# Optimization experiments

Hardware: AMD Instinct MI355X
Metric: run time of the kernel (lower is better)

The kernel has to match this reference:

```python
import jax, jax.numpy as jnp
import numpy as np

B, L, D = 4, 2048, 1024
H = 16
HD = D // H  # head_dim = 64
BASE = 10000.0


def rope_cos_sin(seq_len, head_dim, dtype=jnp.float32):
    inv_freq = 1.0 / (BASE ** (jnp.arange(0, head_dim, 2, dtype=jnp.float32) / head_dim))
    t = jnp.arange(seq_len, dtype=jnp.float32)
    freqs = jnp.outer(t, inv_freq)  # [L, HD/2]
    return jnp.cos(freqs).astype(dtype), jnp.sin(freqs).astype(dtype)


def apply_rope(x, cos, sin):
    # x: [B, H, L, HD]; cos/sin: [L, HD/2]
    x1 = x[..., ::2]
    x2 = x[..., 1::2]
    c = cos[None, None, :, :]
    s = sin[None, None, :, :]
    # NOTE: original concatenates halves (does not re-interleave)
    return jnp.concatenate([x1 * c - x2 * s, x1 * s + x2 * c], axis=-1)


def setup_inputs() -> dict:
    key = jax.random.key(0)
    k1, k2, k3 = jax.random.split(key, 3)
    x = jax.random.normal(k1, (B, L, D), dtype=jnp.float32)
    W_qkv = jax.random.normal(k2, (3 * D, D), dtype=jnp.float32) * (D ** -0.5)
    W_proj = jax.random.normal(k3, (D, D), dtype=jnp.float32) * (D ** -0.5)
    return {"x": x, "W_qkv": W_qkv, "W_proj": W_proj}


def reference(x, W_qkv, W_proj):
    b, l, d = x.shape
    scale = HD ** -0.5
    qkv = jnp.einsum('bld,ed->ble', x, W_qkv)            # [B, L, 3D]
    qkv = qkv.reshape(b, l, 3, H, HD)
    q, k, v = (jnp.transpose(qkv[:, :, i], (0, 2, 1, 3)) for i in range(3))  # [B,H,L,HD]
    cos, sin = rope_cos_sin(l, HD, x.dtype)
    q = apply_rope(q, cos, sin)
    k = apply_rope(k, cos, sin)
    attn = jnp.einsum('bhqd,bhkd->bhqk', q, k) * scale   # [B,H,L,L]
    attn = jax.nn.softmax(attn, axis=-1)
    out = jnp.einsum('bhqk,bhkd->bhqd', attn, v)         # [B,H,L,HD]
    out = jnp.transpose(out, (0, 2, 1, 3)).reshape(b, l, d)
    return jnp.einsum('bld,ed->ble', out, W_proj)
```

## Files before the change

kernel.cpp:

```cpp
#include <hip/hip_runtime.h>
#include <hip/hip_bf16.h>

typedef unsigned short u16;
typedef unsigned int u32;
typedef __attribute__((ext_vector_type(8))) short bf16x8;
typedef __attribute__((ext_vector_type(4))) float f32x4;

#define NL 2048
#define NH 16

__device__ __forceinline__ float bf2f(u16 v) {
    union { float f; unsigned u; } x; x.u = ((unsigned)v) << 16; return x.f;
}
__device__ __forceinline__ u16 f2bf(float f) {
    union { __hip_bfloat16 h; u16 u; } x; x.h = __float2bfloat16(f); return x.u;
}
__device__ __forceinline__ u32 pk2(float a, float b) {
    union { float f; u32 u; } x, y; x.f = a; y.f = b;
    return ((x.u + 0x8000u) >> 16) | ((y.u + 0x8000u) & 0xffff0000u);
}
__device__ __forceinline__ u32 pkt(float lo, float hi) {
    union { float f; u32 u; } x, y; x.f = lo; y.f = hi;
    return __builtin_amdgcn_perm(y.u, x.u, 0x07060302u);
}
#if __has_builtin(__builtin_amdgcn_exp2f)
#define EXP2F(x) __builtin_amdgcn_exp2f(x)
#else
#define EXP2F(x) __expf((x) * 0.69314718056f)
#endif

__device__ __forceinline__ void gload_lds16(const u16* g, u16* l) {
    __builtin_amdgcn_global_load_lds(
        (__attribute__((address_space(1))) void*)(g),
        (__attribute__((address_space(3))) void*)(l), 16, 0, 0);
}

__global__ __launch_bounds__(256) void cast_all_k(const float* __restrict__ x,
                                                  const float* __restrict__ wq,
                                                  const float* __restrict__ wp,
                                                  u16* __restrict__ xo,
                                                  u16* __restrict__ wqo,
                                                  u16* __restrict__ wpo) {
    int i = blockIdx.x * 256 + threadIdx.x;
    const float* src; u16* dst; int off;
    if (i < 2097152)      { src = x;  dst = xo;  off = i; }
    else if (i < 2883584) { src = wq; dst = wqo; off = i - 2097152; }
    else                  { src = wp; dst = wpo; off = i - 2883584; }
    float4 v = *(const float4*)&src[(size_t)off * 4];
    u16 tmp[4] = {f2bf(v.x), f2bf(v.y), f2bf(v.z), f2bf(v.w)};
    *(ushort4*)&dst[(size_t)off * 4] = *(ushort4*)tmp;
}

__global__ __launch_bounds__(256) void rope_table_k(float* __restrict__ cosT,
                                                    float* __restrict__ sinT) {
    int idx = blockIdx.x * 256 + threadIdx.x;
    int l = idx >> 5, i = idx & 31;
    float invf = exp2f(-(float)i * 0.41524101186092029f);
    float ang = (float)l * invf;
    cosT[idx] = cosf(ang);
    sinT[idx] = sinf(ang);
}

template <typename OutT>
__global__ __launch_bounds__(256) void gemm_bt(const u16* __restrict__ A,
                                               const u16* __restrict__ Bm,
                                               OutT* __restrict__ C,
                                               int M, int N, int K) {
    __shared__ u16 As[128][64];
    __shared__ u16 Bs[128][64];
    const int t = threadIdx.x;
    const int lane = t & 63, wave = t >> 6;
    const int quad = lane >> 4, lrow = lane & 15;
    const int wr = wave >> 1, wc = wave & 1;
    const size_t m0 = (size_t)blockIdx.y * 128, n0 = (size_t)blockIdx.x * 128;

    const int srow = wave * 32 + (lane >> 3);
    const int scg  = (lane & 7) ^ (lane >> 3);

    f32x4 acc[4][4];
#pragma unroll
    for (int i = 0; i < 4; ++i)
#pragma unroll
        for (int j = 0; j < 4; ++j) acc[i][j] = (f32x4)0.0f;

    for (int k0 = 0; k0 < K; k0 += 64) {
#pragma unroll
        for (int j = 0; j < 4; ++j) {
            gload_lds16(&A[(m0 + srow + j * 8) * K + k0 + scg * 8],
                        &As[wave * 32 + j * 8][0]);
            gload_lds16(&Bm[(n0 + srow + j * 8) * K + k0 + scg * 8],
                        &Bs[wave * 32 + j * 8][0]);
        }
        __syncthreads();
#pragma unroll
        for (int ks = 0; ks < 2; ++ks) {
            bf16x8 av[4], bv[4];
#pragma unroll
            for (int i = 0; i < 4; ++i)
                av[i] = *(const bf16x8*)
                    &As[wr * 64 + i * 16 + lrow][(((ks << 2) | quad) ^ (lrow & 7)) << 3];
#pragma unroll
            for (int j = 0; j < 4; ++j)
                bv[j] = *(const bf16x8*)
                    &Bs[wc * 64 + j * 16 + lrow][(((ks << 2) | quad) ^ (lrow & 7)) << 3];
#pragma unroll
            for (int i = 0; i < 4; ++i)
#pragma unroll
                for (int j = 0; j < 4; ++j)
                    acc[i][j] = __builtin_amdgcn_mfma_f32_16x16x32_bf16(
                        av[i], bv[j], acc[i][j], 0, 0, 0);
        }
        __syncthreads();
    }
#pragma unroll
    for (int i = 0; i < 4; ++i)
#pragma unroll
        for (int r = 0; r < 4; ++r) {
            size_t row = m0 + wr * 64 + i * 16 + quad * 4 + r;
#pragma unroll
            for (int j = 0; j < 4; ++j) {
                size_t col = n0 + wc * 64 + j * 16 + lrow;
                if constexpr (sizeof(OutT) == 4)
                    C[row * N + col] = acc[i][j][r];
                else
                    C[row * N + col] = f2bf(acc[i][j][r]);
            }
        }
}

__global__ __launch_bounds__(256) void rope_vt_k(const u16* __restrict__ qkv,
                                                 const float* __restrict__ cosT,
                                                 const float* __restrict__ sinT,
                                                 u16* __restrict__ Q,
                                                 u16* __restrict__ Ko,
                                                 u16* __restrict__ VT) {
    __shared__ u16 vtile[64][72];
    const int lt = blockIdx.x, bh = blockIdx.y;
    const int b = bh >> 4, h = bh & 15;
    const int l0 = lt * 64;
    const int t = threadIdx.x;
    const float SC = 0.180336879f;
#pragma unroll
    for (int c = 0; c < 2; ++c) {
        int flat8 = c * 256 + t;
        int li = flat8 >> 3, dg = flat8 & 7;
        const u16* rowp = qkv + (size_t)(b * NL + l0 + li) * 3072 + h * 64 + dg * 8;
        uint4 qv = *(const uint4*)rowp;
        uint4 kv = *(const uint4*)(rowp + 1024);
        uint4 vv = *(const uint4*)(rowp + 2048);
        *(uint4*)&vtile[li][dg * 8] = vv;
        float4 cs = *(const float4*)&cosT[(l0 + li) * 32 + dg * 4];
        float4 sn = *(const float4*)&sinT[(l0 + li) * 32 + dg * 4];
        union { float f; u32 u; } w;
        float e0, o0, e1, o1, e2, o2, e3, o3;
        w.u = qv.x << 16; e0 = w.f; w.u = qv.x & 0xffff0000u; o0 = w.f;
        w.u = qv.y << 16; e1 = w.f; w.u = qv.y & 0xffff0000u; o1 = w.f;
        w.u = qv.z << 16; e2 = w.f; w.u = qv.z & 0xffff0000u; o2 = w.f;
        w.u = qv.w << 16; e3 = w.f; w.u = qv.w & 0xffff0000u; o3 = w.f;
        float c0 = cs.x * SC, c1 = cs.y * SC, c2 = cs.z * SC, c3 = cs.w * SC;
        float s0 = sn.x * SC, s1 = sn.y * SC, s2 = sn.z * SC, s3 = sn.w * SC;
        size_t ob = ((size_t)(b * NH + h) * NL + l0 + li) * 64;
        *(uint2*)&Q[ob + dg * 4] =
            make_uint2(pk2(e0 * c0 - o0 * s0, e1 * c1 - o1 * s1),
                       pk2(e2 * c2 - o2 * s2, e3 * c3 - o3 * s3));
        *(uint2*)&Q[ob + 32 + dg * 4] =
            make_uint2(pk2(e0 * s0 + o0 * c0, e1 * s1 + o1 * c1),
                       pk2(e2 * s2 + o2 * c2, e3 * s3 + o3 * c3));
        float f0, g0, f1, g1, f2, g2, f3, g3;
        w.u = kv.x << 16; f0 = w.f; w.u = kv.x & 0xffff0000u; g0 = w.f;
        w.u = kv.y << 16; f1 = w.f; w.u = kv.y & 0xffff0000u; g1 = w.f;
        w.u = kv.z << 16; f2 = w.f; w.u = kv.z & 0xffff0000u; g2 = w.f;
        w.u = kv.w << 16; f3 = w.f; w.u = kv.w & 0xffff0000u; g3 = w.f;
        *(uint2*)&Ko[ob + dg * 4] =
            make_uint2(pk2(f0 * cs.x - g0 * sn.x, f1 * cs.y - g1 * sn.y),
                       pk2(f2 * cs.z - g2 * sn.z, f3 * cs.w - g3 * sn.w));
        *(uint2*)&Ko[ob + 32 + dg * 4] =
            make_uint2(pk2(f0 * sn.x + g0 * cs.x, f1 * sn.y + g1 * cs.y),
                       pk2(f2 * sn.z + g2 * cs.z, f3 * sn.w + g3 * cs.w));
    }
    __syncthreads();
#pragma unroll
    for (int c = 0; c < 2; ++c) {
        int flat8 = c * 256 + t;
        int d = flat8 >> 3, lg = flat8 & 7;
        u16 tmp[8];
#pragma unroll
        for (int e = 0; e < 8; ++e) tmp[e] = vtile[lg * 8 + e][d];
        *(uint4*)&VT[((size_t)(bh * 64 + d)) * NL + l0 + lg * 8] = *(uint4*)tmp;
    }
}

__global__ __launch_bounds__(512, 6) void attn_k(const u16* __restrict__ Q,
                                                 const u16* __restrict__ Kg,
                                                 const u16* __restrict__ VT,
                                                 u16* __restrict__ Og) {
    __shared__ __align__(16) char smem[49152];
    u16 (*KsB)[64][64] = (u16(*)[64][64])(smem);
    u16 (*VsB)[64][64] = (u16(*)[64][64])(smem + 16384);
    u16* PsBase = (u16*)(smem + 32768);
    const int t = threadIdx.x;
    const int lane = t & 63, wave = t >> 6;
    const int quad = lane >> 4, lq = lane & 15;
    u16* PsW = PsBase + wave * 1024;

    const int qt = blockIdx.x, bh = blockIdx.y;
    const int q0 = qt * 128;
    const size_t qkbase = (size_t)bh * NL * 64;

    const int rsub = lane >> 3;
    const int scg  = (lane & 7) ^ rsub;

    u16 (*Qtmp)[64] = (u16(*)[64])(smem + 32768);
#pragma unroll
    for (int j = 0; j < 2; ++j)
        gload_lds16(&Q[qkbase + (size_t)(q0 + wave * 16 + j * 8 + rsub) * 64 + scg * 8],
                    &Qtmp[wave * 16 + j * 8][0]);
    const u16* kptr = Kg + qkbase + (size_t)(wave * 8 + rsub) * 64 + scg * 8;
    const u16* vptr = VT + qkbase + (size_t)(wave * 8 + rsub) * NL + scg * 8;
    gload_lds16(kptr, &KsB[0][wave * 8][0]);
    gload_lds16(vptr, &VsB[0][wave * 8][0]);
    kptr += 64 * 64;
    vptr += 64;
    __syncthreads();
    bf16x8 bq[2];
#pragma unroll
    for (int ks = 0; ks < 2; ++ks)
        bq[ks] = *(const bf16x8*)&Qtmp[wave * 16 + lq][(((ks << 2) | quad) ^ (lq & 7)) << 3];

    const bf16x8 ones = (bf16x8)(short)16256;
    f32x4 ot[4];
#pragma unroll
    for (int mt = 0; mt < 4; ++mt) ot[mt] = (f32x4)0.0f;
    f32x4 lacc = (f32x4)0.0f;

    for (int kc = 0; kc < NL / 64; ++kc) {
        __syncthreads();
        if (kc < NL / 64 - 1) {
            gload_lds16(kptr, &KsB[(kc + 1) & 1][wave * 8][0]);
            gload_lds16(vptr, &VsB[(kc + 1) & 1][wave * 8][0]);
            kptr += 64 * 64;
            vptr += 64;
        }
        const int cur = kc & 1;

        f32x4 st[4];
#pragma unroll
        for (int mt = 0; mt < 4; ++mt) st[mt] = (f32x4)0.0f;
#pragma unroll
        for (int ks = 0; ks < 2; ++ks)
#pragma unroll
            for (int mt = 0; mt < 4; ++mt) {
                bf16x8 ak = *(const bf16x8*)
                    &KsB[cur][mt * 16 + lq][(((ks << 2) | quad) ^ (lq & 7)) << 3];
                st[mt] = __builtin_amdgcn_mfma_f32_16x16x32_bf16(ak, bq[ks], st[mt], 0, 0, 0);
            }

#pragma unroll
        for (int mt = 0; mt < 4; ++mt) {
            int pblk = (mt * 2 + (quad >> 1)) ^ (lq & 7);
            *(uint2*)&PsW[lq * 64 + pblk * 8 + (quad & 1) * 4] =
                make_uint2(pkt(EXP2F(st[mt][0]), EXP2F(st[mt][1])),
                           pkt(EXP2F(st[mt][2]), EXP2F(st[mt][3])));
        }
        __builtin_amdgcn_s_waitcnt(0xc07f);

#pragma unroll
        for (int ks = 0; ks < 2; ++ks) {
            bf16x8 bp = *(const bf16x8*)
                &PsW[lq * 64 + ((((ks << 2) | quad)) ^ (lq & 7)) * 8];
            lacc = __builtin_amdgcn_mfma_f32_16x16x32_bf16(ones, bp, lacc, 0, 0, 0);
#pragma unroll
            for (int mt = 0; mt < 4; ++mt) {
                bf16x8 av = *(const bf16x8*)
                    &VsB[cur][mt * 16 + lq][(((ks << 2) | quad) ^ (lq & 7)) << 3];
                ot[mt] = __builtin_amdgcn_mfma_f32_16x16x32_bf16(av, bp, ot[mt], 0, 0, 0);
            }
        }
    }

    __syncthreads();
    float* OT_ls = (float*)(smem + wave * 4352);
    float* Ls_ls = (float*)(smem + 34816);
#pragma unroll
    for (int mt = 0; mt < 4; ++mt)
#pragma unroll
        for (int r = 0; r < 4; ++r)
            OT_ls[(mt * 16 + quad * 4 + r) * 17 + lq] = ot[mt][r];
    if (quad == 0) Ls_ls[wave * 16 + lq] = lacc[0];
    __builtin_amdgcn_s_waitcnt(0xc07f);

    const int qq = lane >> 2, dblk = lane & 3;
    float rls = 1.0f / Ls_ls[wave * 16 + qq];
    u16 tmp[16];
#pragma unroll
    for (int e = 0; e < 16; ++e)
        tmp[e] = f2bf(OT_ls[(dblk * 16 + e) * 17 + qq] * rls);
    const int b = bh >> 4, h = bh & 15;
    size_t orow = (size_t)b * NL + q0 + wave * 16 + qq;
    size_t obase = orow * 1024 + h * 64 + dblk * 16;
    *(uint4*)&Og[obase] = *(uint4*)&tmp[0];
    *(uint4*)&Og[obase + 8] = *(uint4*)&tmp[8];
}

extern "C" void kernel_launch(void* const* d_in, const int* in_sizes, int n_in,
                              void* d_out, int out_size, void* d_ws, size_t ws_size,
                              hipStream_t stream) {
    const float* x     = (const float*)d_in[0];
    const float* Wqkv  = (const float*)d_in[1];
    const float* Wproj = (const float*)d_in[2];
    float* out = (float*)d_out;

    char* ws = (char*)d_ws;
    u16* qkv     = (u16*)ws;
    u16* attnout = (u16*)ws;
    u16* Qw      = (u16*)(ws + 50331648);
    u16* Kw      = (u16*)(ws + 67108864);
    u16* VTw     = (u16*)(ws + 83886080);
    float* cosT  = (float*)(ws + 100663296);
    float* sinT  = (float*)(ws + 100925440);
    u16* x_bf    = (u16*)(ws + 101187584);
    u16* Wqkv_bf = (u16*)(ws + 117964800);
    u16* Wproj_bf= (u16*)(ws + 124256256);

    rope_table_k<<<256, 256, 0, stream>>>(cosT, sinT);
    cast_all_k<<<12288, 256, 0, stream>>>(x, Wqkv, Wproj, x_bf, Wqkv_bf, Wproj_bf);
    gemm_bt<u16><<<dim3(24, 64), 256, 0, stream>>>(x_bf, Wqkv_bf, qkv, 8192, 3072, 1024);
    rope_vt_k<<<dim3(32, 64), 256, 0, stream>>>(qkv, cosT, sinT, Qw, Kw, VTw);
    attn_k<<<dim3(16, 64), 512, 0, stream>>>(Qw, Kw, VTw, attnout);
    gemm_bt<float><<<dim3(8, 64), 256, 0, stream>>>(attnout, Wproj_bf, out, 8192, 1024, 1024);
}
```

Measured before the change: 280.1 us.

## Process two query tiles per wave in attention to reuse K/V fragments

Each wave now handles 32 query rows as two 16-row halves instead of 16 rows. Each K and V fragment read from LDS feeds MFMAs for both halves, which halves LDS traffic per MFMA and halves the number of K/V tiles streamed per query. The query tile per block doubles to 256, so the grid shrinks to 512 blocks. LDS grows to 64KB and the launch-bound occupancy hint drops from 6 to 4, which may reduce latency hiding and CU balance.

```diff
diff --git a/kernel.cpp b/kernel.cpp
--- a/kernel.cpp
+++ b/kernel.cpp
@@ -190,21 +190,21 @@
     }
 }
 
-__global__ __launch_bounds__(512, 6) void attn_k(const u16* __restrict__ Q,
+__global__ __launch_bounds__(512, 4) void attn_k(const u16* __restrict__ Q,
                                                  const u16* __restrict__ Kg,
                                                  const u16* __restrict__ VT,
                                                  u16* __restrict__ Og) {
-    __shared__ __align__(16) char smem[49152];
+    __shared__ __align__(16) char smem[65536];
     u16 (*KsB)[64][64] = (u16(*)[64][64])(smem);
     u16 (*VsB)[64][64] = (u16(*)[64][64])(smem + 16384);
     u16* PsBase = (u16*)(smem + 32768);
     const int t = threadIdx.x;
     const int lane = t & 63, wave = t >> 6;
     const int quad = lane >> 4, lq = lane & 15;
-    u16* PsW = PsBase + wave * 1024;
+    u16* PsW = PsBase + wave * 2048;
 
     const int qt = blockIdx.x, bh = blockIdx.y;
-    const int q0 = qt * 128;
+    const int q0 = qt * 256;
     const size_t qkbase = (size_t)bh * NL * 64;
 
     const int rsub = lane >> 3;
@@ -212,9 +212,9 @@
 
     u16 (*Qtmp)[64] = (u16(*)[64])(smem + 32768);
 #pragma unroll
-    for (int j = 0; j < 2; ++j)
-        gload_lds16(&Q[qkbase + (size_t)(q0 + wave * 16 + j * 8 + rsub) * 64 + scg * 8],
-                    &Qtmp[wave * 16 + j * 8][0]);
+    for (int j = 0; j < 4; ++j)
+        gload_lds16(&Q[qkbase + (size_t)(q0 + wave * 32 + j * 8 + rsub) * 64 + scg * 8],
+                    &Qtmp[wave * 32 + j * 8][0]);
     const u16* kptr = Kg + qkbase + (size_t)(wave * 8 + rsub) * 64 + scg * 8;
     const u16* vptr = VT + qkbase + (size_t)(wave * 8 + rsub) * NL + scg * 8;
     gload_lds16(kptr, &KsB[0][wave * 8][0]);
@@ -222,16 +222,21 @@
     kptr += 64 * 64;
     vptr += 64;
     __syncthreads();
-    bf16x8 bq[2];
-#pragma unroll
-    for (int ks = 0; ks < 2; ++ks)
-        bq[ks] = *(const bf16x8*)&Qtmp[wave * 16 + lq][(((ks << 2) | quad) ^ (lq & 7)) << 3];
+    bf16x8 bq[2][2];
+#pragma unroll
+    for (int qh = 0; qh < 2; ++qh)
+#pragma unroll
+        for (int ks = 0; ks < 2; ++ks)
+            bq[qh][ks] = *(const bf16x8*)
+                &Qtmp[wave * 32 + qh * 16 + lq][(((ks << 2) | quad) ^ (lq & 7)) << 3];
 
     const bf16x8 ones = (bf16x8)(short)16256;
-    f32x4 ot[4];
-#pragma unroll
-    for (int mt = 0; mt < 4; ++mt) ot[mt] = (f32x4)0.0f;
-    f32x4 lacc = (f32x4)0.0f;
+    f32x4 ot[2][4];
+#pragma unroll
+    for (int qh = 0; qh < 2; ++qh)
+#pragma unroll
+        for (int mt = 0; mt < 4; ++mt) ot[qh][mt] = (f32x4)0.0f;
+    f32x4 lacc[2] = {(f32x4)0.0f, (f32x4)0.0f};
 
     for (int kc = 0; kc < NL / 64; ++kc) {
         __syncthreads();
@@ -243,37 +248,45 @@
         }
         const int cur = kc & 1;
 
-        f32x4 st[4];
-#pragma unroll
-        for (int mt = 0; mt < 4; ++mt) st[mt] = (f32x4)0.0f;
+        f32x4 st[2][4];
+#pragma unroll
+        for (int qh = 0; qh < 2; ++qh)
+#pragma unroll
+            for (int mt = 0; mt < 4; ++mt) st[qh][mt] = (f32x4)0.0f;
 #pragma unroll
         for (int ks = 0; ks < 2; ++ks)
 #pragma unroll
             for (int mt = 0; mt < 4; ++mt) {
                 bf16x8 ak = *(const bf16x8*)
                     &KsB[cur][mt * 16 + lq][(((ks << 2) | quad) ^ (lq & 7)) << 3];
-                st[mt] = __builtin_amdgcn_mfma_f32_16x16x32_bf16(ak, bq[ks], st[mt], 0, 0, 0);
+                st[0][mt] = __builtin_amdgcn_mfma_f32_16x16x32_bf16(ak, bq[0][ks], st[0][mt], 0, 0, 0);
+                st[1][mt] = __builtin_amdgcn_mfma_f32_16x16x32_bf16(ak, bq[1][ks], st[1][mt], 0, 0, 0);
             }
 
 #pragma unroll
-        for (int mt = 0; mt < 4; ++mt) {
-            int pblk = (mt * 2 + (quad >> 1)) ^ (lq & 7);
-            *(uint2*)&PsW[lq * 64 + pblk * 8 + (quad & 1) * 4] =
-                make_uint2(pkt(EXP2F(st[mt][0]), EXP2F(st[mt][1])),
-                           pkt(EXP2F(st[mt][2]), EXP2F(st[mt][3])));
-        }
+        for (int qh = 0; qh < 2; ++qh)
+#pragma unroll
+            for (int mt = 0; mt < 4; ++mt) {
+                int pblk = (mt * 2 + (quad >> 1)) ^ (lq & 7);
+                *(uint2*)&PsW[(qh * 16 + lq) * 64 + pblk * 8 + (quad & 1) * 4] =
+                    make_uint2(pkt(EXP2F(st[qh][mt][0]), EXP2F(st[qh][mt][1])),
+                               pkt(EXP2F(st[qh][mt][2]), EXP2F(st[qh][mt][3])));
+            }
         __builtin_amdgcn_s_waitcnt(0xc07f);
 
 #pragma unroll
         for (int ks = 0; ks < 2; ++ks) {
-            bf16x8 bp = *(const bf16x8*)
-                &PsW[lq * 64 + ((((ks << 2) | quad)) ^ (lq & 7)) * 8];
-            lacc = __builtin_amdgcn_mfma_f32_16x16x32_bf16(ones, bp, lacc, 0, 0, 0);
+            const int sw = (((ks << 2) | quad) ^ (lq & 7)) * 8;
+            bf16x8 bp0 = *(const bf16x8*)&PsW[lq * 64 + sw];
+            bf16x8 bp1 = *(const bf16x8*)&PsW[(16 + lq) * 64 + sw];
+            lacc[0] = __builtin_amdgcn_mfma_f32_16x16x32_bf16(ones, bp0, lacc[0], 0, 0, 0);
+            lacc[1] = __builtin_amdgcn_mfma_f32_16x16x32_bf16(ones, bp1, lacc[1], 0, 0, 0);
 #pragma unroll
             for (int mt = 0; mt < 4; ++mt) {
                 bf16x8 av = *(const bf16x8*)
                     &VsB[cur][mt * 16 + lq][(((ks << 2) | quad) ^ (lq & 7)) << 3];
-                ot[mt] = __builtin_amdgcn_mfma_f32_16x16x32_bf16(av, bp, ot[mt], 0, 0, 0);
+                ot[0][mt] = __builtin_amdgcn_mfma_f32_16x16x32_bf16(av, bp0, ot[0][mt], 0, 0, 0);
+                ot[1][mt] = __builtin_amdgcn_mfma_f32_16x16x32_bf16(av, bp1, ot[1][mt], 0, 0, 0);
             }
         }
     }
@@ -281,25 +294,28 @@
     __syncthreads();
     float* OT_ls = (float*)(smem + wave * 4352);
     float* Ls_ls = (float*)(smem + 34816);
-#pragma unroll
-    for (int mt = 0; mt < 4; ++mt)
-#pragma unroll
-        for (int r = 0; r < 4; ++r)
-            OT_ls[(mt * 16 + quad * 4 + r) * 17 + lq] = ot[mt][r];
-    if (quad == 0) Ls_ls[wave * 16 + lq] = lacc[0];
-    __builtin_amdgcn_s_waitcnt(0xc07f);
-
+    const int b = bh >> 4, h = bh & 15;
     const int qq = lane >> 2, dblk = lane & 3;
-    float rls = 1.0f / Ls_ls[wave * 16 + qq];
-    u16 tmp[16];
-#pragma unroll
-    for (int e = 0; e < 16; ++e)
-        tmp[e] = f2bf(OT_ls[(dblk * 16 + e) * 17 + qq] * rls);
-    const int b = bh >> 4, h = bh & 15;
-    size_t orow = (size_t)b * NL + q0 + wave * 16 + qq;
-    size_t obase = orow * 1024 + h * 64 + dblk * 16;
-    *(uint4*)&Og[obase] = *(uint4*)&tmp[0];
-    *(uint4*)&Og[obase + 8] = *(uint4*)&tmp[8];
+#pragma unroll
+    for (int qh = 0; qh < 2; ++qh) {
+#pragma unroll
+        for (int mt = 0; mt < 4; ++mt)
+#pragma unroll
+            for (int r = 0; r < 4; ++r)
+                OT_ls[(mt * 16 + quad * 4 + r) * 17 + lq] = ot[qh][mt][r];
+        if (quad == 0) Ls_ls[wave * 16 + lq] = lacc[qh][0];
+        __builtin_amdgcn_s_waitcnt(0xc07f);
+
+        float rls = 1.0f / Ls_ls[wave * 16 + qq];
+        u16 tmp[16];
+#pragma unroll
+        for (int e = 0; e < 16; ++e)
+            tmp[e] = f2bf(OT_ls[(dblk * 16 + e) * 17 + qq] * rls);
+        size_t orow = (size_t)b * NL + q0 + wave * 32 + qh * 16 + qq;
+        size_t obase = orow * 1024 + h * 64 + dblk * 16;
+        *(uint4*)&Og[obase] = *(uint4*)&tmp[0];
+        *(uint4*)&Og[obase + 8] = *(uint4*)&tmp[8];
+    }
 }
 
 extern "C" void kernel_launch(void* const* d_in, const int* in_sizes, int n_in,
@@ -326,6 +342,6 @@
     cast_all_k<<<12288, 256, 0, stream>>>(x, Wqkv, Wproj, x_bf, Wqkv_bf, Wproj_bf);
     gemm_bt<u16><<<dim3(24, 64), 256, 0, stream>>>(x_bf, Wqkv_bf, qkv, 8192, 3072, 1024);
     rope_vt_k<<<dim3(32, 64), 256, 0, stream>>>(qkv, cosT, sinT, Qw, Kw, VTw);
-    attn_k<<<dim3(16, 64), 512, 0, stream>>>(Qw, Kw, VTw, attnout);
+    attn_k<<<dim3(8, 64), 512, 0, stream>>>(Qw, Kw, VTw, attnout);
     gemm_bt<float><<<dim3(8, 64), 256, 0, stream>>>(attnout, Wproj_bf, out, 8192, 1024, 1024);
 }
```

Measured after the change: 266.5 us. 4.9% less time.
